# Optimization experiments

Hardware: AMD Instinct MI355X
Metric: run time of the kernel (lower is better)

## Reference

```python
import jax, jax.numpy as jnp
import numpy as np

N = 50000      # nodes
E = 640000     # edges
D = 128        # input/hidden dim
L = 3          # GIN layers
G = 256        # graphs in batch
LAT = 64       # latent dim
BN_EPS = 1e-5
SLOPE = 0.2    # LeakyReLU negative slope


def _leaky(h):
    return jnp.where(h >= 0, h, SLOPE * h)


def setup_inputs() -> dict:
    key = jax.random.key(0)
    ks = jax.random.split(key, 8)
    x = jax.random.normal(ks[0], (N, D), dtype=jnp.float32)
    edge_index = jax.random.randint(ks[1], (2, E), 0, N, dtype=jnp.int64)
    batch = jnp.sort(jax.random.randint(ks[2], (N,), 0, G, dtype=jnp.int64))
    W1 = jax.random.normal(ks[3], (L, D, D), dtype=jnp.float32) * 0.05
    W2 = jax.random.normal(ks[4], (L, D, D), dtype=jnp.float32) * 0.05
    fc_W = jax.random.normal(ks[5], (LAT, D), dtype=jnp.float32) * 0.05
    return {
        "x": x,
        "W1": W1,
        "b1": jnp.zeros((L, D), jnp.float32),
        "bn_g": jnp.ones((L, D), jnp.float32),
        "bn_b": jnp.zeros((L, D), jnp.float32),
        "bn_m": jnp.zeros((L, D), jnp.float32),
        "bn_v": jax.random.uniform(ks[6], (L, D), jnp.float32, 0.5, 1.5),
        "W2": W2,
        "b2": jnp.zeros((L, D), jnp.float32),
        "out_g": jnp.ones((D,), jnp.float32),
        "out_b": jnp.zeros((D,), jnp.float32),
        "out_m": jnp.zeros((D,), jnp.float32),
        "out_v": jax.random.uniform(ks[7], (D,), jnp.float32, 0.5, 1.5),
        "fc_W": fc_W,
        "fc_b": jnp.zeros((LAT,), jnp.float32),
        "edge_index": edge_index,
        "batch": batch,
    }


def reference(x, W1, b1, bn_g, bn_b, bn_m, bn_v, W2, b2,
              out_g, out_b, out_m, out_v, fc_W, fc_b,
              edge_index, batch):
    src, dst = edge_index[0], edge_index[1]
    for i in range(L):
        # GINConv: (1+eps)*x + sum_{j in N(i)} x_j  (eps=0 default)
        agg = x + jax.ops.segment_sum(x[src], dst, num_segments=N)
        # MLP: Linear -> LeakyReLU -> BatchNorm(eval) -> Linear -> LeakyReLU
        h = _leaky(agg @ W1[i].T + b1[i])
        h = (h - bn_m[i]) * jax.lax.rsqrt(bn_v[i] + BN_EPS) * bn_g[i] + bn_b[i]
        x = _leaky(h @ W2[i].T + b2[i])
        # dropout is identity in eval mode
    pooled = jax.ops.segment_sum(x, batch, num_segments=G)  # [G, D]
    out = (pooled - out_m) * jax.lax.rsqrt(out_v + BN_EPS) * out_g + out_b
    return out @ fc_W.T + fc_b  # [G, LAT]
```

## Files before the change

### kernel.cpp

```cpp
#include <hip/hip_runtime.h>
#include <cstdint>
#include <cstddef>

#define NN 50000
#define EE 640000
#define DD 128
#define LL 3
#define GG 256
#define LATD 64

typedef __attribute__((ext_vector_type(8))) __bf16 bf16x8;
typedef __attribute__((ext_vector_type(4))) float f32x4;

__device__ __forceinline__ unsigned short f2bf(float f) {
  __bf16 h = (__bf16)f;
  return __builtin_bit_cast(unsigned short, h);
}
__device__ __forceinline__ float bf2f(unsigned int u16) {
  unsigned int x = u16 << 16;
  return __builtin_bit_cast(float, x);
}
__device__ __forceinline__ void unpack8(uint4 v, float* f) {
  f[0] = bf2f(v.x & 0xffffu); f[1] = bf2f(v.x >> 16);
  f[2] = bf2f(v.y & 0xffffu); f[3] = bf2f(v.y >> 16);
  f[4] = bf2f(v.z & 0xffffu); f[5] = bf2f(v.z >> 16);
  f[6] = bf2f(v.w & 0xffffu); f[7] = bf2f(v.w >> 16);
}
__device__ __forceinline__ void acc8(uint4 v, float* f) {
  f[0] += bf2f(v.x & 0xffffu); f[1] += bf2f(v.x >> 16);
  f[2] += bf2f(v.y & 0xffffu); f[3] += bf2f(v.y >> 16);
  f[4] += bf2f(v.z & 0xffffu); f[5] += bf2f(v.z >> 16);
  f[6] += bf2f(v.w & 0xffffu); f[7] += bf2f(v.w >> 16);
}
__device__ __forceinline__ uint4 pack8(const float* f) {
  uint4 v;
  v.x = f2bf(f[0]) | ((unsigned)f2bf(f[1]) << 16);
  v.y = f2bf(f[2]) | ((unsigned)f2bf(f[3]) << 16);
  v.z = f2bf(f[4]) | ((unsigned)f2bf(f[5]) << 16);
  v.w = f2bf(f[6]) | ((unsigned)f2bf(f[7]) << 16);
  return v;
}

#define SWZ(byte_, row_) ((byte_) ^ (((row_) & 7) << 4))
#define CPAD 4

#define CVT_BLK 3125
#define WCV_BLK 48
#define HIST_BLK 2500
__global__ __launch_bounds__(256) void prep_kernel(
    const float4* __restrict__ x, uint4* __restrict__ xb,
    const float* __restrict__ W1, const float* __restrict__ W2,
    uint4* __restrict__ wb, const int* __restrict__ dst,
    int* __restrict__ counts) {
  int b = blockIdx.x;
  if (b < CVT_BLK) {
    int t = b * 256 + threadIdx.x;
    float4 a = x[t * 2], bb = x[t * 2 + 1];
    float f[8] = {a.x, a.y, a.z, a.w, bb.x, bb.y, bb.z, bb.w};
    xb[t] = pack8(f);
  } else if (b < CVT_BLK + WCV_BLK) {
    int t = (b - CVT_BLK) * 256 + threadIdx.x;
    int m = t >> 11;
    int q = t & 2047;
    int byte = q * 16;
    int row = byte >> 8;
    int inner = byte & 255;
    int isrc = inner ^ ((row & 7) << 4);
    int k0 = isrc >> 1;
    const float* Wsrc = (m & 1) ? W2 : W1;
    const float* p = Wsrc + ((size_t)(m >> 1) * DD * DD + row * DD + k0);
    float4 f0 = ((const float4*)p)[0], f1 = ((const float4*)p)[1];
    float f[8] = {f0.x, f0.y, f0.z, f0.w, f1.x, f1.y, f1.z, f1.w};
    wb[(size_t)m * 2048 + q] = pack8(f);
  } else {
    int e = (b - CVT_BLK - WCV_BLK) * 256 + threadIdx.x;
    atomicAdd(&counts[dst[e] << CPAD], 1);
  }
}

__global__ __launch_bounds__(256) void scan1_kernel(const int* __restrict__ counts,
                                                    int* __restrict__ rp,
                                                    int* __restrict__ bsum, int n) {
  int i = blockIdx.x * 256 + threadIdx.x;
  int v = (i < n) ? counts[i << CPAD] : 0;
  int lane = threadIdx.x & 63, w = threadIdx.x >> 6;
  int s = v;
#pragma unroll
  for (int off = 1; off < 64; off <<= 1) {
    int u = __shfl_up(s, off);
    if (lane >= off) s += u;
  }
  __shared__ int ws[4];
  if (lane == 63) ws[w] = s;
  __syncthreads();
  int add = 0;
#pragma unroll
  for (int k = 0; k < 4; ++k) if (k < w) add += ws[k];
  int incl = s + add;
  if (i < n) rp[i] = incl - v;
  if (threadIdx.x == 255) bsum[blockIdx.x] = incl;
}

__global__ __launch_bounds__(256) void scan2_kernel(int* __restrict__ bsum, int nb) {
  int t = threadIdx.x;
  int v = (t < nb) ? bsum[t] : 0;
  int lane = t & 63, w = t >> 6;
  int s = v;
#pragma unroll
  for (int off = 1; off < 64; off <<= 1) {
    int u = __shfl_up(s, off);
    if (lane >= off) s += u;
  }
  __shared__ int ws[4];
  if (lane == 63) ws[w] = s;
  __syncthreads();
  int add = 0;
#pragma unroll
  for (int k = 0; k < 4; ++k) if (k < w) add += ws[k];
  int incl = s + add;
  if (t < nb) bsum[t] = incl - v;
}

__global__ __launch_bounds__(256) void scan3_kernel(int* __restrict__ rp,
                                                    int* __restrict__ cursor,
                                                    const int* __restrict__ bsum, int n) {
  int i = blockIdx.x * 256 + threadIdx.x;
  if (i < n) {
    int v = rp[i] + bsum[blockIdx.x];
    rp[i] = v;
    cursor[i << CPAD] = v;
  }
  if (i == 0) rp[n] = EE;
}

__global__ __launch_bounds__(256) void fill_kernel(const int* __restrict__ src,
                                                   const int* __restrict__ dst,
                                                   int* __restrict__ cursor,
                                                   int* __restrict__ col, int E) {
  int e = blockIdx.x * blockDim.x + threadIdx.x;
  if (e < E) {
    int p = atomicAdd(&cursor[dst[e] << CPAD], 1);
    col[p] = src[e];
  }
}

__global__ __launch_bounds__(256, 4) void agg_kernel(const uint4* __restrict__ xin,
                                                     const int* __restrict__ row_ptr,
                                                     const int* __restrict__ colv,
                                                     uint4* __restrict__ agg, int n) {
  int tid = blockIdx.x * 256 + threadIdx.x;
  int node = tid >> 4;
  int c = tid & 15;
  if (node >= n) return;
  float acc[8];
  unpack8(xin[(size_t)node * 16 + c], acc);
  int s = row_ptr[node], e = row_ptr[node + 1];
  int j = s;
  for (; j + 8 <= e; j += 8) {
    int i0 = colv[j],     i1 = colv[j + 1], i2 = colv[j + 2], i3 = colv[j + 3];
    int i4 = colv[j + 4], i5 = colv[j + 5], i6 = colv[j + 6], i7 = colv[j + 7];
    uint4 v0 = xin[(size_t)i0 * 16 + c];
    uint4 v1 = xin[(size_t)i1 * 16 + c];
    uint4 v2 = xin[(size_t)i2 * 16 + c];
    uint4 v3 = xin[(size_t)i3 * 16 + c];
    uint4 v4 = xin[(size_t)i4 * 16 + c];
    uint4 v5 = xin[(size_t)i5 * 16 + c];
    uint4 v6 = xin[(size_t)i6 * 16 + c];
    uint4 v7 = xin[(size_t)i7 * 16 + c];
    acc8(v0, acc); acc8(v1, acc); acc8(v2, acc); acc8(v3, acc);
    acc8(v4, acc); acc8(v5, acc); acc8(v6, acc); acc8(v7, acc);
  }
  for (; j + 2 <= e; j += 2) {
    uint4 v0 = xin[(size_t)colv[j] * 16 + c];
    uint4 v1 = xin[(size_t)colv[j + 1] * 16 + c];
    acc8(v0, acc); acc8(v1, acc);
  }
  if (j < e) acc8(xin[(size_t)colv[j] * 16 + c], acc);
  agg[(size_t)node * 16 + c] = pack8(acc);
}

__global__ __launch_bounds__(512) void mlp_nb(
    const uint4* __restrict__ aggb, uint4* __restrict__ xout,
    const uint4* __restrict__ w1b, const uint4* __restrict__ w2b,
    const float* __restrict__ b1, const float* __restrict__ bng,
    const float* __restrict__ bnb, const float* __restrict__ bnm,
    const float* __restrict__ bnv, const float* __restrict__ b2) {
  __shared__ __align__(16) char smem[98304];
  char* w1p = smem;
  char* w2p = smem + 32768;
#pragma unroll
  for (int it = 0; it < 8; ++it) {
    int q = it * 512 + threadIdx.x;
    ((uint4*)w1p)[q] = w1b[q];
    ((uint4*)w2p)[q] = w2b[q];
  }
  int lane = threadIdx.x & 63;
  int c = lane & 15;
  int kq = lane >> 4;
  int wave = threadIdx.x >> 6;
  char* hs = smem + 65536 + wave * 4096;
  __syncthreads();

  float b1v[8], sv[8], tv[8], b2v[8];
#pragma unroll
  for (int ni = 0; ni < 8; ++ni) {
    int cc = ni * 16 + c;
    b1v[ni] = b1[cc];
    float s = bng[cc] * rsqrtf(bnv[cc] + 1e-5f);
    sv[ni] = s;
    tv[ni] = bnb[cc] - bnm[cc] * s;
    b2v[ni] = b2[cc];
  }

  for (int t = blockIdx.x * 8 + wave; t < NN / 16; t += 2048) {
    int base = t * 16;
    f32x4 acc[8];
#pragma unroll
    for (int ni = 0; ni < 8; ++ni) acc[ni] = (f32x4){0.f, 0.f, 0.f, 0.f};

#pragma unroll
    for (int ks = 0; ks < 4; ++ks) {
      bf16x8 a = *(const bf16x8*)(aggb + (size_t)(base + c) * 16 + ks * 4 + kq);
#pragma unroll
      for (int ni = 0; ni < 8; ++ni) {
        int wr = ni * 16 + c;
        bf16x8 bfr = *(const bf16x8*)(w1p + SWZ(wr * 256 + ks * 64 + kq * 16, wr));
        acc[ni] = __builtin_amdgcn_mfma_f32_16x16x32_bf16(a, bfr, acc[ni], 0, 0, 0);
      }
    }

#pragma unroll
    for (int ni = 0; ni < 8; ++ni)
#pragma unroll
      for (int r = 0; r < 4; ++r) {
        float h = acc[ni][r] + b1v[ni];
        h = h >= 0.f ? h : 0.2f * h;
        h = h * sv[ni] + tv[ni];
        int row = kq * 4 + r;
        *(__bf16*)(hs + row * 256 + SWZ((ni * 16 + c) * 2, row)) = (__bf16)h;
      }

#pragma unroll
    for (int ni = 0; ni < 8; ++ni) acc[ni] = (f32x4){0.f, 0.f, 0.f, 0.f};

#pragma unroll
    for (int ks = 0; ks < 4; ++ks) {
      bf16x8 a = *(const bf16x8*)(hs + c * 256 + SWZ(ks * 64 + kq * 16, c));
#pragma unroll
      for (int ni = 0; ni < 8; ++ni) {
        int wr = ni * 16 + c;
        bf16x8 bfr = *(const bf16x8*)(w2p + SWZ(wr * 256 + ks * 64 + kq * 16, wr));
        acc[ni] = __builtin_amdgcn_mfma_f32_16x16x32_bf16(a, bfr, acc[ni], 0, 0, 0);
      }
    }

#pragma unroll
    for (int ni = 0; ni < 8; ++ni)
#pragma unroll
      for (int r = 0; r < 4; ++r) {
        float xo = acc[ni][r] + b2v[ni];
        xo = xo >= 0.f ? xo : 0.2f * xo;
        int row = kq * 4 + r;
        *(__bf16*)(hs + row * 256 + (ni * 16 + c) * 2) = (__bf16)xo;
      }
#pragma unroll
    for (int it2 = 0; it2 < 4; ++it2) {
      int chunk = it2 * 64 + lane;
      uint4 v = *(const uint4*)(hs + chunk * 16);
      xout[(size_t)base * 16 + chunk] = v;
    }
  }
}

__global__ __launch_bounds__(128) void head_kernel(
    const unsigned short* __restrict__ x, const int* __restrict__ batch,
    const float* __restrict__ og, const float* __restrict__ ob,
    const float* __restrict__ om, const float* __restrict__ ov,
    const float* __restrict__ fcW, const float* __restrict__ fcb,
    float* __restrict__ out) {
  __shared__ float pb[DD];
  __shared__ int slo, shi;
  int g = blockIdx.x;
  int t = threadIdx.x;
  if (t == 0) {
    int lo = 0, hi = NN;
    while (lo < hi) { int m = (lo + hi) >> 1; if (batch[m] < g) lo = m + 1; else hi = m; }
    slo = lo;
    lo = 0; hi = NN;
    while (lo < hi) { int m = (lo + hi) >> 1; if (batch[m] < g + 1) lo = m + 1; else hi = m; }
    shi = lo;
  }
  __syncthreads();
  float acc = 0.f;
  int node = slo;
  for (; node + 4 <= shi; node += 4) {
    float a0 = bf2f(x[(size_t)(node + 0) * DD + t]);
    float a1 = bf2f(x[(size_t)(node + 1) * DD + t]);
    float a2 = bf2f(x[(size_t)(node + 2) * DD + t]);
    float a3 = bf2f(x[(size_t)(node + 3) * DD + t]);
    acc += (a0 + a1) + (a2 + a3);
  }
  for (; node < shi; ++node) acc += bf2f(x[(size_t)node * DD + t]);
  float s = og[t] * rsqrtf(ov[t] + 1e-5f);
  pb[t] = (acc - om[t]) * s + ob[t];
  __syncthreads();
  if (t < LATD) {
    float a = fcb[t];
#pragma unroll 8
    for (int d = 0; d < DD; ++d) a = fmaf(fcW[t * DD + d], pb[d], a);
    out[(size_t)g * LATD + t] = a;
  }
}

extern "C" void kernel_launch(void* const* d_in, const int* in_sizes, int n_in,
                              void* d_out, int out_size, void* d_ws, size_t ws_size,
                              hipStream_t stream) {
  const float* x   = (const float*)d_in[0];
  const float* W1  = (const float*)d_in[1];
  const float* b1  = (const float*)d_in[2];
  const float* bng = (const float*)d_in[3];
  const float* bnb = (const float*)d_in[4];
  const float* bnm = (const float*)d_in[5];
  const float* bnv = (const float*)d_in[6];
  const float* W2  = (const float*)d_in[7];
  const float* b2  = (const float*)d_in[8];
  const float* og  = (const float*)d_in[9];
  const float* ob  = (const float*)d_in[10];
  const float* om  = (const float*)d_in[11];
  const float* ov  = (const float*)d_in[12];
  const float* fcW = (const float*)d_in[13];
  const float* fcb = (const float*)d_in[14];
  const int* ei    = (const int*)d_in[15];
  const int* batch = (const int*)d_in[16];
  const int* src  = ei;
  const int* dstp = ei + EE;

  char* ws = (char*)d_ws;
  size_t off = 0;
  auto alloc = [&](size_t bytes) {
    void* p = ws + off;
    off += (bytes + 255) & ~(size_t)255;
    return p;
  };
  unsigned short* xb0  = (unsigned short*)alloc((size_t)NN * DD * 2);
  unsigned short* xb1  = (unsigned short*)alloc((size_t)NN * DD * 2);
  unsigned short* aggb = (unsigned short*)alloc((size_t)NN * DD * 2);
  uint4* wb     = (uint4*)alloc((size_t)6 * 2048 * 16);
  int* row_ptr  = (int*)alloc((NN + 1) * 4);
  int* cursor   = (int*)alloc((size_t)NN * 64);
  int* counts   = (int*)alloc((size_t)NN * 64);
  int* col      = (int*)alloc(EE * 4);
  int* bsum     = (int*)alloc(256 * 4);

  hipMemsetAsync(counts, 0, (size_t)NN * 64, stream);

  prep_kernel<<<CVT_BLK + WCV_BLK + HIST_BLK, 256, 0, stream>>>(
      (const float4*)x, (uint4*)xb0, W1, W2, wb, dstp, counts);

  const int NB = (NN + 255) / 256;
  scan1_kernel<<<NB, 256, 0, stream>>>(counts, row_ptr, bsum, NN);
  scan2_kernel<<<1, 256, 0, stream>>>(bsum, NB);
  scan3_kernel<<<NB, 256, 0, stream>>>(row_ptr, cursor, bsum, NN);
  fill_kernel<<<(EE + 255) / 256, 256, 0, stream>>>(src, dstp, cursor, col, EE);

  unsigned short* xcur = xb0;
  unsigned short* xnext = xb1;
  for (int i = 0; i < LL; ++i) {
    agg_kernel<<<(NN * 16 + 255) / 256, 256, 0, stream>>>(
        (const uint4*)xcur, row_ptr, col, (uint4*)aggb, NN);
    mlp_nb<<<256, 512, 0, stream>>>(
        (const uint4*)aggb, (uint4*)xnext,
        wb + (size_t)i * 4096, wb + (size_t)i * 4096 + 2048,
        b1 + i * DD, bng + i * DD, bnb + i * DD, bnm + i * DD, bnv + i * DD,
        b2 + i * DD);
    unsigned short* t = xcur; xcur = xnext; xnext = t;
  }
  head_kernel<<<GG, 128, 0, stream>>>(
      xcur, batch, og, ob, om, ov, fcW, fcb, (float*)d_out);
}
```

Baseline: 219.9 us.

## Fuse CSR build and prep kernels into one cooperative kernel with grid syncs

```diff
diff --git a/kernel.cpp b/kernel.cpp
--- a/kernel.cpp
+++ b/kernel.cpp
@@ -1,6 +1,9 @@
 #include <hip/hip_runtime.h>
+#include <hip/hip_cooperative_groups.h>
 #include <cstdint>
 #include <cstddef>
+
+namespace cg = cooperative_groups;
 
 #define NN 50000
 #define EE 640000
@@ -44,24 +47,28 @@
 #define SWZ(byte_, row_) ((byte_) ^ (((row_) & 7) << 4))
 #define CPAD 4
 
-#define CVT_BLK 3125
-#define WCV_BLK 48
-#define HIST_BLK 2500
-__global__ __launch_bounds__(256) void prep_kernel(
+__global__ __launch_bounds__(256, 4) void build_kernel(
     const float4* __restrict__ x, uint4* __restrict__ xb,
     const float* __restrict__ W1, const float* __restrict__ W2,
-    uint4* __restrict__ wb, const int* __restrict__ dst,
-    int* __restrict__ counts) {
+    uint4* __restrict__ wb,
+    const int* __restrict__ src, const int* __restrict__ dstp,
+    int* __restrict__ counts, int* __restrict__ rp,
+    int* __restrict__ cursor, int* __restrict__ col,
+    int* __restrict__ bsum) {
+  cg::grid_group grid = cg::this_grid();
+  __shared__ int ws[4];
   int b = blockIdx.x;
-  if (b < CVT_BLK) {
-    int t = b * 256 + threadIdx.x;
+  int tid = b * 256 + (int)threadIdx.x;
+  int lane = threadIdx.x & 63, w = threadIdx.x >> 6;
+
+  for (int t = tid; t < NN * DD / 8; t += 262144) {
     float4 a = x[t * 2], bb = x[t * 2 + 1];
     float f[8] = {a.x, a.y, a.z, a.w, bb.x, bb.y, bb.z, bb.w};
     xb[t] = pack8(f);
-  } else if (b < CVT_BLK + WCV_BLK) {
-    int t = (b - CVT_BLK) * 256 + threadIdx.x;
-    int m = t >> 11;
-    int q = t & 2047;
+  }
+  if (tid < 12288) {
+    int m = tid >> 11;
+    int q = tid & 2047;
     int byte = q * 16;
     int row = byte >> 8;
     int inner = byte & 255;
@@ -72,74 +79,65 @@
     float4 f0 = ((const float4*)p)[0], f1 = ((const float4*)p)[1];
     float f[8] = {f0.x, f0.y, f0.z, f0.w, f1.x, f1.y, f1.z, f1.w};
     wb[(size_t)m * 2048 + q] = pack8(f);
-  } else {
-    int e = (b - CVT_BLK - WCV_BLK) * 256 + threadIdx.x;
-    atomicAdd(&counts[dst[e] << CPAD], 1);
-  }
-}
-
-__global__ __launch_bounds__(256) void scan1_kernel(const int* __restrict__ counts,
-                                                    int* __restrict__ rp,
-                                                    int* __restrict__ bsum, int n) {
-  int i = blockIdx.x * 256 + threadIdx.x;
-  int v = (i < n) ? counts[i << CPAD] : 0;
-  int lane = threadIdx.x & 63, w = threadIdx.x >> 6;
-  int s = v;
-#pragma unroll
-  for (int off = 1; off < 64; off <<= 1) {
-    int u = __shfl_up(s, off);
-    if (lane >= off) s += u;
-  }
-  __shared__ int ws[4];
-  if (lane == 63) ws[w] = s;
-  __syncthreads();
-  int add = 0;
-#pragma unroll
-  for (int k = 0; k < 4; ++k) if (k < w) add += ws[k];
-  int incl = s + add;
-  if (i < n) rp[i] = incl - v;
-  if (threadIdx.x == 255) bsum[blockIdx.x] = incl;
-}
-
-__global__ __launch_bounds__(256) void scan2_kernel(int* __restrict__ bsum, int nb) {
-  int t = threadIdx.x;
-  int v = (t < nb) ? bsum[t] : 0;
-  int lane = t & 63, w = t >> 6;
-  int s = v;
-#pragma unroll
-  for (int off = 1; off < 64; off <<= 1) {
-    int u = __shfl_up(s, off);
-    if (lane >= off) s += u;
-  }
-  __shared__ int ws[4];
-  if (lane == 63) ws[w] = s;
-  __syncthreads();
-  int add = 0;
-#pragma unroll
-  for (int k = 0; k < 4; ++k) if (k < w) add += ws[k];
-  int incl = s + add;
-  if (t < nb) bsum[t] = incl - v;
-}
-
-__global__ __launch_bounds__(256) void scan3_kernel(int* __restrict__ rp,
-                                                    int* __restrict__ cursor,
-                                                    const int* __restrict__ bsum, int n) {
-  int i = blockIdx.x * 256 + threadIdx.x;
-  if (i < n) {
-    int v = rp[i] + bsum[blockIdx.x];
-    rp[i] = v;
-    cursor[i << CPAD] = v;
-  }
-  if (i == 0) rp[n] = EE;
-}
-
-__global__ __launch_bounds__(256) void fill_kernel(const int* __restrict__ src,
-                                                   const int* __restrict__ dst,
-                                                   int* __restrict__ cursor,
-                                                   int* __restrict__ col, int E) {
-  int e = blockIdx.x * blockDim.x + threadIdx.x;
-  if (e < E) {
-    int p = atomicAdd(&cursor[dst[e] << CPAD], 1);
+  }
+  for (int e = tid; e < EE; e += 262144) {
+    atomicAdd(&counts[dstp[e] << CPAD], 1);
+  }
+  grid.sync();
+
+  if (b < 196) {
+    int i = b * 256 + (int)threadIdx.x;
+    int v = (i < NN) ? counts[i << CPAD] : 0;
+    int s = v;
+#pragma unroll
+    for (int off = 1; off < 64; off <<= 1) {
+      int u = __shfl_up(s, off);
+      if (lane >= off) s += u;
+    }
+    if (lane == 63) ws[w] = s;
+    __syncthreads();
+    int add = 0;
+#pragma unroll
+    for (int k = 0; k < 4; ++k) if (k < w) add += ws[k];
+    int incl = s + add;
+    if (i < NN) rp[i] = incl - v;
+    if (threadIdx.x == 255) bsum[b] = incl;
+  }
+  grid.sync();
+
+  if (b == 0) {
+    int t = threadIdx.x;
+    int v = (t < 196) ? bsum[t] : 0;
+    int s = v;
+#pragma unroll
+    for (int off = 1; off < 64; off <<= 1) {
+      int u = __shfl_up(s, off);
+      if (lane >= off) s += u;
+    }
+    __syncthreads();
+    if (lane == 63) ws[w] = s;
+    __syncthreads();
+    int add = 0;
+#pragma unroll
+    for (int k = 0; k < 4; ++k) if (k < w) add += ws[k];
+    int incl = s + add;
+    if (t < 196) bsum[t] = incl - v;
+  }
+  grid.sync();
+
+  if (b < 196) {
+    int i = b * 256 + (int)threadIdx.x;
+    if (i < NN) {
+      int v = rp[i] + bsum[b];
+      rp[i] = v;
+      cursor[i << CPAD] = v;
+    }
+    if (i == 0) rp[NN] = EE;
+  }
+  grid.sync();
+
+  for (int e = tid; e < EE; e += 262144) {
+    int p = atomicAdd(&cursor[dstp[e] << CPAD], 1);
     col[p] = src[e];
   }
 }
@@ -332,7 +330,7 @@
   const float* fcb = (const float*)d_in[14];
   const int* ei    = (const int*)d_in[15];
   const int* batch = (const int*)d_in[16];
-  const int* src  = ei;
+  const int* srcp = ei;
   const int* dstp = ei + EE;
 
   char* ws = (char*)d_ws;
@@ -354,14 +352,17 @@
 
   hipMemsetAsync(counts, 0, (size_t)NN * 64, stream);
 
-  prep_kernel<<<CVT_BLK + WCV_BLK + HIST_BLK, 256, 0, stream>>>(
-      (const float4*)x, (uint4*)xb0, W1, W2, wb, dstp, counts);
-
-  const int NB = (NN + 255) / 256;
-  scan1_kernel<<<NB, 256, 0, stream>>>(counts, row_ptr, bsum, NN);
-  scan2_kernel<<<1, 256, 0, stream>>>(bsum, NB);
-  scan3_kernel<<<NB, 256, 0, stream>>>(row_ptr, cursor, bsum, NN);
-  fill_kernel<<<(EE + 255) / 256, 256, 0, stream>>>(src, dstp, cursor, col, EE);
+  {
+    const float4* x4 = (const float4*)x;
+    uint4* xb0u = (uint4*)xb0;
+    void* args[] = {
+      (void*)&x4, (void*)&xb0u, (void*)&W1, (void*)&W2, (void*)&wb,
+      (void*)&srcp, (void*)&dstp, (void*)&counts, (void*)&row_ptr,
+      (void*)&cursor, (void*)&col, (void*)&bsum
+    };
+    hipLaunchCooperativeKernel((const void*)build_kernel, dim3(1024), dim3(256),
+                               args, 0, stream);
+  }
 
   unsigned short* xcur = xb0;
   unsigned short* xnext = xb1;
```

Result: slower. 625.6 us (+184.6%).
